# Performance work log

Measured on AMD Instinct MI355X. Metric: run time of the kernel, lower is better.

The kernel has to match this reference:

```python
import jax, jax.numpy as jnp
import numpy as np

B, T, D_IN, H = 128, 1024, 64, 512
EPS = 1e-5


def _layernorm(x, gamma, beta):
    mu = jnp.mean(x, axis=-1, keepdims=True)
    var = jnp.mean(jnp.square(x - mu), axis=-1, keepdims=True)
    return (x - mu) * jax.lax.rsqrt(var + EPS) * gamma + beta


def setup_inputs() -> dict:
    key = jax.random.key(0)
    ks = jax.random.split(key, 10)
    s_in = 1.0 / np.sqrt(D_IN)
    s_h = 1.0 / np.sqrt(H)
    return {
        "x": jax.random.normal(ks[0], (B, T, D_IN), dtype=jnp.float32),
        # layer 0: input_dim -> hidden
        "Wi0": jax.random.uniform(ks[1], (D_IN, H), jnp.float32, -s_in, s_in),
        "bi0": jax.random.uniform(ks[2], (H,), jnp.float32, -s_in, s_in),
        "Wh0": jax.random.uniform(ks[3], (H, H), jnp.float32, -s_h, s_h),
        "bh0": jax.random.uniform(ks[4], (H,), jnp.float32, -s_h, s_h),
        "g0": jnp.ones((H,), jnp.float32),
        "be0": jnp.zeros((H,), jnp.float32),
        # layer 1: hidden -> hidden
        "Wi1": jax.random.uniform(ks[5], (H, H), jnp.float32, -s_h, s_h),
        "bi1": jax.random.uniform(ks[6], (H,), jnp.float32, -s_h, s_h),
        "Wh1": jax.random.uniform(ks[7], (H, H), jnp.float32, -s_h, s_h),
        "bh1": jax.random.uniform(ks[8], (H,), jnp.float32, -s_h, s_h),
        "g1": jnp.ones((H,), jnp.float32),
        "be1": jnp.zeros((H,), jnp.float32),
        # output head: hidden -> 1
        "Wfc": jax.random.uniform(ks[9], (H, 1), jnp.float32, -s_h, s_h),
        "bfc": jnp.zeros((1,), jnp.float32),
    }


def reference(x, Wi0, bi0, Wh0, bh0, g0, be0, Wi1, bi1, Wh1, bh1, g1, be1, Wfc, bfc):
    def step(carry, x_t):
        h0, h1 = carry
        # layer 0: tanh(x W + h W) + residual + LayerNorm
        cand0 = jnp.tanh(x_t @ Wi0 + bi0 + h0 @ Wh0 + bh0)
        h0n = _layernorm(cand0 + h0, g0, be0)
        # layer 1
        cand1 = jnp.tanh(h0n @ Wi1 + bi1 + h1 @ Wh1 + bh1)
        h1n = _layernorm(cand1 + h1, g1, be1)
        return (h0n, h1n), None

    h_init = (jnp.zeros((x.shape[0], Wh0.shape[0]), x.dtype),
              jnp.zeros((x.shape[0], Wh1.shape[0]), x.dtype))
    xs = jnp.swapaxes(x, 0, 1)  # [T, B, D]
    (h0, h1), _ = jax.lax.scan(step, h_init, xs)
    return h1 @ Wfc + bfc  # [B, 1]
```

## Files before the change

### kernel.cpp

```cpp
#include <hip/hip_runtime.h>


#define T_SZ 1024
#define DD   64
#define HH   512
#define NCH  8
#define NBLK 16

typedef __attribute__((ext_vector_type(8))) short short8;
typedef __attribute__((ext_vector_type(4))) float f32x4;
typedef unsigned long long ull;

__device__ __forceinline__ unsigned short f2b(float f) {
  unsigned u = __float_as_uint(f);
  u += 0x7fffu + ((u >> 16) & 1u);
  return (unsigned short)(u >> 16);
}
__device__ __forceinline__ float b2f(unsigned short s) {
  return __uint_as_float(((unsigned)s) << 16);
}
__device__ __forceinline__ ull packf2(float a, float b) {
  return (ull)__float_as_uint(a) | ((ull)__float_as_uint(b) << 32);
}
__device__ __forceinline__ float unpack_lo(ull u) { return __uint_as_float((unsigned)u); }
__device__ __forceinline__ float unpack_hi(ull u) { return __uint_as_float((unsigned)(u >> 32)); }
__device__ __forceinline__ void st_rlx(ull* p, ull v) {
  __hip_atomic_store(p, v, __ATOMIC_RELAXED, __HIP_MEMORY_SCOPE_AGENT);
}
__device__ __forceinline__ ull ld_rlx(const ull* p) {
  return __hip_atomic_load(p, __ATOMIC_RELAXED, __HIP_MEMORY_SCOPE_AGENT);
}
__device__ __forceinline__ unsigned ld_flag(const unsigned* p) {
  return __hip_atomic_load(p, __ATOMIC_RELAXED, __HIP_MEMORY_SCOPE_AGENT);
}
__device__ __forceinline__ void st_flag(unsigned* p, unsigned v) {
  asm volatile("" ::: "memory");
  __hip_atomic_store(p, v, __ATOMIC_RELAXED, __HIP_MEMORY_SCOPE_AGENT);
}
__device__ __forceinline__ float fast_tanh(float z) {
  const float e = __builtin_amdgcn_exp2f(z * 2.885390081777927f);
  return 1.f - 2.f * __builtin_amdgcn_rcpf(e + 1.f);
}

__global__ void prep_kernel(const float* __restrict__ Wh0, const float* __restrict__ Wi1,
                            const float* __restrict__ Wh1,
                            const float* __restrict__ bi0, const float* __restrict__ bh0,
                            const float* __restrict__ bi1, const float* __restrict__ bh1,
                            const float* __restrict__ g0, const float* __restrict__ be0,
                            const float* __restrict__ g1, const float* __restrict__ be1,
                            float* __restrict__ cvec, unsigned* __restrict__ flags) {
  int g = blockIdx.x * blockDim.x + threadIdx.x;
  if (g < HH) {
    float uw0 = 0.f, qw0 = 0.f, uw1 = 0.f, qw1 = 0.f, uh1 = 0.f, qh1 = 0.f;
    for (int j = 0; j < HH; ++j) {
      float a = Wh0[j * HH + g], b = Wi1[j * HH + g], d = Wh1[j * HH + g];
      uw0 += g0[j] * a; qw0 += be0[j] * a;
      uw1 += g0[j] * b; qw1 += be0[j] * b;
      uh1 += g1[j] * d; qh1 += be1[j] * d;
    }
    float b0 = bi0[g] + bh0[g], b1 = bi1[g] + bh1[g];
    cvec[0 * HH + g] = b0 + qw0;
    cvec[1 * HH + g] = b0;
    cvec[2 * HH + g] = b1 + qw1 + qh1;
    cvec[3 * HH + g] = b1 + qw1;
    cvec[4 * HH + g] = uw0;
    cvec[5 * HH + g] = uw1;
    cvec[6 * HH + g] = uh1;
  }
  if (g < 4096) flags[g] = 0;
}

__global__ __launch_bounds__(512, 1) void rnn_mfma(
    const float* __restrict__ x,
    const float* __restrict__ Wi0, const float* __restrict__ Wh0,
    const float* __restrict__ Wi1, const float* __restrict__ Wh1,
    const float* __restrict__ cvec,
    const float* __restrict__ g0v, const float* __restrict__ be0v,
    const float* __restrict__ g1v, const float* __restrict__ be1v,
    const float* __restrict__ wfc, const float* __restrict__ bfc,
    ull* __restrict__ pay, ull* __restrict__ pst,
    unsigned* __restrict__ flags, float* __restrict__ out) {

  const int blk = blockIdx.x, group = blk >> 4, p = blk & 15;
  const int tid = threadIdx.x;
  const int wave = tid >> 6, lane = tid & 63;
  const int quad = lane >> 4, m16 = lane & 15;

  __shared__ unsigned short a0bf[16][536];
  __shared__ unsigned short a1bf[16][536];
  __shared__ unsigned short xsb[16][72];
  __shared__ float partsA[8][8][33];
  __shared__ float partsB[8][8][33];
  __shared__ float partsC[8][8][33];
  __shared__ float partsX[2][8][33];
  __shared__ float2 st0[NCH][NBLK];
  __shared__ float2 st1[NCH][NBLK];

  for (int i = tid; i < 16 * 536; i += 512) {
    (&a0bf[0][0])[i] = 0; (&a1bf[0][0])[i] = 0;
  }
  for (int i = tid; i < 16 * 72; i += 512) (&xsb[0][0])[i] = 0;
  if (tid < NCH * NBLK) {
    (&st0[0][0])[tid] = make_float2(0.f, 0.f);
    (&st1[0][0])[tid] = make_float2(0.f, 0.f);
  }
  {
    float xv = x[((size_t)(group * NCH + wave) * T_SZ) * DD + lane];
    xsb[wave][lane] = f2b(xv);
  }

  short8 wf0[2][2], wfA[2][2], wfB[2][2], wfx[2];
#pragma unroll
  for (int n = 0; n < 2; ++n)
#pragma unroll
    for (int j = 0; j < 8; ++j) wfx[n][j] = 0;
#pragma unroll
  for (int sl = 0; sl < 2; ++sl)
#pragma unroll
    for (int n = 0; n < 2; ++n) {
      const int col = p * 32 + n * 16 + m16;
#pragma unroll
      for (int j = 0; j < 8; ++j) {
        const int k = wave * 64 + sl * 32 + quad * 8 + j;
        wf0[sl][n][j] = (short)f2b(g0v[k] * Wh0[(size_t)k * HH + col]);
        wfA[sl][n][j] = (short)f2b(g0v[k] * Wi1[(size_t)k * HH + col]);
        wfB[sl][n][j] = (short)f2b(g1v[k] * Wh1[(size_t)k * HH + col]);
      }
    }
  if (wave < 2) {
#pragma unroll
    for (int n = 0; n < 2; ++n) {
      const int col = p * 32 + n * 16 + m16;
#pragma unroll
      for (int j = 0; j < 8; ++j)
        wfx[n][j] = (short)f2b(Wi0[(size_t)(wave * 32 + quad * 8 + j) * HH + col]);
    }
  }

  const int cl    = lane & 31;
  const int ech   = ((wave & 3) << 1) + (lane >> 5);
  const int col_e = p * 32 + cl;
  const float c0f = cvec[col_e],          c0i = cvec[HH + col_e];
  const float c1f = cvec[2 * HH + col_e], c1i = cvec[3 * HH + col_e];
  const float uw0 = cvec[4 * HH + col_e], uw1 = cvec[5 * HH + col_e];
  const float uh1 = cvec[6 * HH + col_e];
  const float g0c = g0v[col_e], be0c = be0v[col_e];
  const float g1c = g1v[col_e], be1c = be1v[col_e];

  const int Lp = (wave >= 4) ? 1 : 0;
  ull* const pubpay0 = pay + ((((size_t)blk * 2 + Lp) * 2 + 0) * NCH + ech) * 8 + (cl >> 2);
  ull* const pubpay1 = pubpay0 + (size_t)NCH * 8;
  ull* const pubpst0 = pst + (((size_t)blk * 2 + Lp) * 2 + 0) * NCH + ech;
  ull* const pubpst1 = pubpst0 + NCH;
  unsigned short* const ep_lds = &((wave < 4) ? a0bf : a1bf)[ech][p * 32 + cl];

  const int j0   = 2 * wave;
  const bool two = (j0 + 1 < 15);
  const int pg0  = j0 + (j0 >= p);
  const int pg1  = two ? ((j0 + 1) + ((j0 + 1) >= p)) : pg0;
  const unsigned* pf0 = flags + (group * NBLK + pg0) * 16;
  const unsigned* pf1 = flags + (group * NBLK + pg1) * 16;

  const ull* gp0[5]; const ull* gp1[5]; ull* glw[5]; bool gv[5], gva0[5];
#pragma unroll
  for (int k = 0; k < 5; ++k) {
    const int li  = lane + (k << 6);
    const int lim = two ? 288 : 144;
    const int jr  = (li >= 144) ? 1 : 0;
    const int r2  = li - 144 * jr;
    const int pl  = jr ? pg1 : pg0;
    gv[k]  = (li < lim);
    gva0[k] = gv[k] && (r2 < 72);
    const int L  = (r2 >= 72) ? 1 : 0;
    const int rr = r2 - 72 * L;
    const size_t pb = ((size_t)(group * NBLK + pl) * 2 + L) * 2;
    if (rr < 64) {
      gp0[k] = pay + ((pb + 0) * NCH + (rr >> 3)) * 8 + (rr & 7);
      gp1[k] = pay + ((pb + 1) * NCH + (rr >> 3)) * 8 + (rr & 7);
      glw[k] = (ull*)&(L ? a1bf : a0bf)[rr >> 3][pl * 32 + 4 * (rr & 7)];
    } else {
      gp0[k] = pst + (pb + 0) * NCH + (rr - 64);
      gp1[k] = pst + (pb + 1) * NCH + (rr - 64);
      glw[k] = (ull*)&(L ? st1 : st0)[rr - 64][pl];
    }
  }

  const float* xptr = x + ((size_t)(group * NCH + wave) * T_SZ + 1) * DD + lane;

  float v2prev0 = 0.f, v2prev1 = 0.f;
  float myS0 = 0.f, myQ0 = 0.f, myS1 = 0.f, myQ1 = 0.f;
  __syncthreads();

  for (int s = 0; s <= T_SZ; ++s) {
    const int par = s & 1;

    float m0 = 0.f, r0 = 0.f, m1p = 0.f, r1p = 0.f;
    if (s > 0) {
      float S = 0.f, Q = 0.f;
#pragma unroll
      for (int i = 0; i < NBLK; ++i) { float2 sq = st0[ech][i]; S += sq.x; Q += sq.y; }
      m0 = S * (1.f / HH);
      r0 = __builtin_amdgcn_rsqf(Q * (1.f / HH) - m0 * m0 + 1e-5f);
    }
    if (wave >= 4 && s > 1) {
      float S = 0.f, Q = 0.f;
#pragma unroll
      for (int i = 0; i < NBLK; ++i) { float2 sq = st1[ech][i]; S += sq.x; Q += sq.y; }
      m1p = S * (1.f / HH);
      r1p = __builtin_amdgcn_rsqf(Q * (1.f / HH) - m1p * m1p + 1e-5f);
    }

    {
      f32x4 aA0 = {0.f,0.f,0.f,0.f}, aA1 = {0.f,0.f,0.f,0.f};
      f32x4 aB0 = {0.f,0.f,0.f,0.f}, aB1 = {0.f,0.f,0.f,0.f};
      f32x4 aC0 = {0.f,0.f,0.f,0.f}, aC1 = {0.f,0.f,0.f,0.f};
#pragma unroll
      for (int sl = 0; sl < 2; ++sl) {
        const short8 af0 = *(const short8*)&a0bf[m16][wave * 64 + sl * 32 + quad * 8];
        const short8 af1 = *(const short8*)&a1bf[m16][wave * 64 + sl * 32 + quad * 8];
        aA0 = __builtin_amdgcn_mfma_f32_16x16x32_bf16(af0, wf0[sl][0], aA0, 0, 0, 0);
        aA1 = __builtin_amdgcn_mfma_f32_16x16x32_bf16(af0, wf0[sl][1], aA1, 0, 0, 0);
        aC0 = __builtin_amdgcn_mfma_f32_16x16x32_bf16(af0, wfA[sl][0], aC0, 0, 0, 0);
        aC1 = __builtin_amdgcn_mfma_f32_16x16x32_bf16(af0, wfA[sl][1], aC1, 0, 0, 0);
        aB0 = __builtin_amdgcn_mfma_f32_16x16x32_bf16(af1, wfB[sl][0], aB0, 0, 0, 0);
        aB1 = __builtin_amdgcn_mfma_f32_16x16x32_bf16(af1, wfB[sl][1], aB1, 0, 0, 0);
      }
      if (lane < 32) {
#pragma unroll
        for (int r = 0; r < 4; ++r) {
          partsA[wave][quad * 4 + r][m16]      = aA0[r];
          partsA[wave][quad * 4 + r][16 + m16] = aA1[r];
          partsB[wave][quad * 4 + r][m16]      = aB0[r];
          partsB[wave][quad * 4 + r][16 + m16] = aB1[r];
          partsC[wave][quad * 4 + r][m16]      = aC0[r];
          partsC[wave][quad * 4 + r][16 + m16] = aC1[r];
        }
      }
      if (wave < 2) {
        f32x4 ax0 = {0.f,0.f,0.f,0.f}, ax1 = {0.f,0.f,0.f,0.f};
        const short8 xf = *(const short8*)&xsb[m16][wave * 32 + quad * 8];
        ax0 = __builtin_amdgcn_mfma_f32_16x16x32_bf16(xf, wfx[0], ax0, 0, 0, 0);
        ax1 = __builtin_amdgcn_mfma_f32_16x16x32_bf16(xf, wfx[1], ax1, 0, 0, 0);
        if (lane < 32) {
#pragma unroll
          for (int r = 0; r < 4; ++r) {
            partsX[wave][quad * 4 + r][m16]      = ax0[r];
            partsX[wave][quad * 4 + r][16 + m16] = ax1[r];
          }
        }
      }
    }
    __syncthreads();

    if (wave < 4) {
      if (s < T_SZ) {
        float sH = 0.f;
#pragma unroll
        for (int w = 0; w < 8; ++w) sH += partsA[w][ech][cl];
        const float sX = partsX[0][ech][cl] + partsX[1][ech][cl];
        const float z = ((s == 0) ? c0i : c0f) + r0 * sH - r0 * m0 * uw0 + sX;
        const float h0prev = (s == 0) ? 0.f : (v2prev0 - m0) * r0 * g0c + be0c;
        const float v2 = fast_tanh(z) + h0prev;
        v2prev0 = v2;
        const unsigned vb = f2b(v2);
        *ep_lds = (unsigned short)vb;
        const unsigned u01 = vb | (__shfl_down(vb, 1) << 16);
        const unsigned u23 = __shfl_down(u01, 2);
        if ((cl & 3) == 0)
          st_rlx((par ? pubpay1 : pubpay0), (ull)u01 | ((ull)u23 << 32));
        float S = v2, Q = v2 * v2;
#pragma unroll
        for (int off = 16; off; off >>= 1) {
          S += __shfl_down(S, off, 32); Q += __shfl_down(Q, off, 32);
        }
        if (cl == 0) {
          myS0 = S; myQ0 = Q;
          st_rlx((par ? pubpst1 : pubpst0), packf2(S, Q));
        }
      }
    } else if (s >= 1) {
      float sB = 0.f, sC = 0.f;
#pragma unroll
      for (int w = 0; w < 8; ++w) { sB += partsB[w][ech][cl]; sC += partsC[w][ech][cl]; }
      const float z = ((s == 1) ? c1i : c1f) + r0 * sC - r0 * m0 * uw1
                      + r1p * sB - r1p * m1p * uh1;
      const float h1prev = (s == 1) ? 0.f : (v2prev1 - m1p) * r1p * g1c + be1c;
      const float v2 = fast_tanh(z) + h1prev;
      v2prev1 = v2;
      const unsigned vb = f2b(v2);
      *ep_lds = (unsigned short)vb;
      const unsigned u01 = vb | (__shfl_down(vb, 1) << 16);
      const unsigned u23 = __shfl_down(u01, 2);
      if ((cl & 3) == 0)
        st_rlx((par ? pubpay1 : pubpay0), (ull)u01 | ((ull)u23 << 32));
      float S = v2, Q = v2 * v2;
#pragma unroll
      for (int off = 16; off; off >>= 1) {
        S += __shfl_down(S, off, 32); Q += __shfl_down(Q, off, 32);
      }
      if (cl == 0) {
        myS1 = S; myQ1 = Q;
        st_rlx((par ? pubpst1 : pubpst0), packf2(S, Q));
      }
    }
    __syncthreads();
    if (tid == 0) st_flag(flags + blk * 16, (unsigned)(s + 1));
    if (s == T_SZ) break;

    if (cl == 0) {
      if (wave < 4)       st0[ech][p] = make_float2(myS0, myQ0);
      else if (s >= 1)    st1[ech][p] = make_float2(myS1, myQ1);
    }
    float xv = 0.f;
    if (s + 1 < T_SZ) xv = *xptr;
    xptr += DD;

    if (two) {
      while (ld_flag(pf0) < (unsigned)(s + 1) || ld_flag(pf1) < (unsigned)(s + 1))
        __builtin_amdgcn_s_sleep(1);
    } else {
      while (ld_flag(pf0) < (unsigned)(s + 1)) __builtin_amdgcn_s_sleep(1);
    }

    {
      ull tv[5];
#pragma unroll
      for (int k = 0; k < 5; ++k) {
        const bool v = s ? gv[k] : gva0[k];
        tv[k] = 0;
        if (v) tv[k] = ld_rlx(par ? gp1[k] : gp0[k]);
      }
#pragma unroll
      for (int k = 0; k < 5; ++k) {
        const bool v = s ? gv[k] : gva0[k];
        if (v) *glw[k] = tv[k];
      }
    }
    if (s + 1 < T_SZ) xsb[wave][lane] = f2b(xv);
    __syncthreads();
  }

  if (p == 0) {
    if (tid < 16) {
      const unsigned* pf = flags + (group * NBLK + tid) * 16;
      while (ld_flag(pf) < (unsigned)(T_SZ + 1)) __builtin_amdgcn_s_sleep(1);
    }
    __syncthreads();
    const int c = wave;
    ull su = 0;
    if (lane < 16)
      su = ld_rlx(pst + (((size_t)(group * NBLK + lane) * 2 + 1) * 2 + 0) * NCH + c);
    float S = unpack_lo(su), Q = unpack_hi(su);
#pragma unroll
    for (int off = 32; off; off >>= 1) { S += __shfl_down(S, off); Q += __shfl_down(Q, off); }
    S = __shfl(S, 0); Q = __shfl(Q, 0);
    const float m1 = S * (1.f / HH);
    const float r1 = 1.f / sqrtf(Q * (1.f / HH) - m1 * m1 + 1e-5f);
    float o = 0.f;
#pragma unroll
    for (int it = 0; it < 2; ++it) {
      const int j2 = lane * 2 + it, pl = j2 >> 3, j = j2 & 7;
      ull u = ld_rlx(pay + ((((size_t)(group * NBLK + pl) * 2 + 1) * 2 + 0) * NCH + c) * 8 + j);
#pragma unroll
      for (int q = 0; q < 4; ++q) {
        const int col = pl * 32 + 4 * j + q;
        const float h = (b2f((unsigned short)(u >> (16 * q))) - m1) * r1 * g1v[col] + be1v[col];
        o += h * wfc[col];
      }
    }
#pragma unroll
    for (int off = 32; off; off >>= 1) o += __shfl_down(o, off);
    if (lane == 0) out[group * NCH + c] = o + bfc[0];
  }
}

extern "C" void kernel_launch(void* const* d_in, const int* in_sizes, int n_in,
                              void* d_out, int out_size, void* d_ws, size_t ws_size,
                              hipStream_t stream) {
  const float* x   = (const float*)d_in[0];
  const float* Wi0 = (const float*)d_in[1];
  const float* bi0 = (const float*)d_in[2];
  const float* Wh0 = (const float*)d_in[3];
  const float* bh0 = (const float*)d_in[4];
  const float* g0  = (const float*)d_in[5];
  const float* be0 = (const float*)d_in[6];
  const float* Wi1 = (const float*)d_in[7];
  const float* bi1 = (const float*)d_in[8];
  const float* Wh1 = (const float*)d_in[9];
  const float* bh1 = (const float*)d_in[10];
  const float* g1  = (const float*)d_in[11];
  const float* be1 = (const float*)d_in[12];
  const float* Wfc = (const float*)d_in[13];
  const float* bfc = (const float*)d_in[14];
  float* out = (float*)d_out;

  char* ws = (char*)d_ws;
  float* cvec     = (float*)(ws);
  ull* pay        = (ull*)(ws + 16384);
  ull* pst        = (ull*)(ws + 16384 + 524288);
  unsigned* flags = (unsigned*)(ws + 16384 + 524288 + 65536);

  prep_kernel<<<256, 256, 0, stream>>>(Wh0, Wi1, Wh1, bi0, bh0, bi1, bh1,
                                       g0, be0, g1, be1, cvec, flags);
  rnn_mfma<<<256, 512, 0, stream>>>(x, Wi0, Wh0, Wi1, Wh1, cvec,
                                    g0, be0, g1, be1, Wfc, bfc,
                                    pay, pst, flags, out);
}
```

Baseline: 3.159 ms.

## Replace step flags with sentinel-valued per-consumer mailboxes for inter-block exchange

Removes the per-step flag counters and the extra __syncthreads before publishing. Each producer now writes its hidden-state payload and LayerNorm stats into 16 per-consumer slots. Consumers poll each slot until it no longer holds a sentinel value, then reset it to the sentinel after reading. The goal is to cut one barrier plus a flag round-trip per timestep, so readiness is detected directly on the data. In exchange each producer issues 16 times as many global stores, the workspace grows, and correctness depends on 64-bit atomic visibility and on real data never equalling the all-ones sentinel.

```diff
diff --git a/kernel.cpp b/kernel.cpp
--- a/kernel.cpp
+++ b/kernel.cpp
@@ -6,6 +6,7 @@
 #define HH   512
 #define NCH  8
 #define NBLK 16
+#define SENT 0xFFFFFFFFFFFFFFFFull
 
 typedef __attribute__((ext_vector_type(8))) short short8;
 typedef __attribute__((ext_vector_type(4))) float f32x4;
@@ -29,13 +30,6 @@
 }
 __device__ __forceinline__ ull ld_rlx(const ull* p) {
   return __hip_atomic_load(p, __ATOMIC_RELAXED, __HIP_MEMORY_SCOPE_AGENT);
-}
-__device__ __forceinline__ unsigned ld_flag(const unsigned* p) {
-  return __hip_atomic_load(p, __ATOMIC_RELAXED, __HIP_MEMORY_SCOPE_AGENT);
-}
-__device__ __forceinline__ void st_flag(unsigned* p, unsigned v) {
-  asm volatile("" ::: "memory");
-  __hip_atomic_store(p, v, __ATOMIC_RELAXED, __HIP_MEMORY_SCOPE_AGENT);
 }
 __device__ __forceinline__ float fast_tanh(float z) {
   const float e = __builtin_amdgcn_exp2f(z * 2.885390081777927f);
@@ -48,7 +42,8 @@
                             const float* __restrict__ bi1, const float* __restrict__ bh1,
                             const float* __restrict__ g0, const float* __restrict__ be0,
                             const float* __restrict__ g1, const float* __restrict__ be1,
-                            float* __restrict__ cvec, unsigned* __restrict__ flags) {
+                            float* __restrict__ cvec,
+                            ull* __restrict__ pay, ull* __restrict__ pst) {
   int g = blockIdx.x * blockDim.x + threadIdx.x;
   if (g < HH) {
     float uw0 = 0.f, qw0 = 0.f, uw1 = 0.f, qw1 = 0.f, uh1 = 0.f, qh1 = 0.f;
@@ -67,7 +62,12 @@
     cvec[5 * HH + g] = uw1;
     cvec[6 * HH + g] = uh1;
   }
-  if (g < 4096) flags[g] = 0;
+  ull* pp = pay + (size_t)g * 16;
+#pragma unroll
+  for (int i = 0; i < 16; ++i) pp[i] = SENT;
+  ull* ps = pst + (size_t)g * 2;
+#pragma unroll
+  for (int i = 0; i < 2; ++i) ps[i] = SENT;
 }
 
 __global__ __launch_bounds__(512, 1) void rnn_mfma(
@@ -79,7 +79,7 @@
     const float* __restrict__ g1v, const float* __restrict__ be1v,
     const float* __restrict__ wfc, const float* __restrict__ bfc,
     ull* __restrict__ pay, ull* __restrict__ pst,
-    unsigned* __restrict__ flags, float* __restrict__ out) {
+    float* __restrict__ out) {
 
   const int blk = blockIdx.x, group = blk >> 4, p = blk & 15;
   const int tid = threadIdx.x;
@@ -148,20 +148,18 @@
   const float g1c = g1v[col_e], be1c = be1v[col_e];
 
   const int Lp = (wave >= 4) ? 1 : 0;
-  ull* const pubpay0 = pay + ((((size_t)blk * 2 + Lp) * 2 + 0) * NCH + ech) * 8 + (cl >> 2);
-  ull* const pubpay1 = pubpay0 + (size_t)NCH * 8;
-  ull* const pubpst0 = pst + (((size_t)blk * 2 + Lp) * 2 + 0) * NCH + ech;
-  ull* const pubpst1 = pubpst0 + NCH;
+  ull* const ppayA = pay + ((((size_t)blk * 2 + Lp) * 2 + 0) * 16) * 64 + ech * 8 + (cl >> 2);
+  ull* const ppayB = pay + ((((size_t)blk * 2 + Lp) * 2 + 1) * 16) * 64 + ech * 8 + (cl >> 2);
+  ull* const ppstA = pst + ((((size_t)blk * 2 + Lp) * 2 + 0) * 16) * 8 + ech;
+  ull* const ppstB = pst + ((((size_t)blk * 2 + Lp) * 2 + 1) * 16) * 8 + ech;
   unsigned short* const ep_lds = &((wave < 4) ? a0bf : a1bf)[ech][p * 32 + cl];
 
   const int j0   = 2 * wave;
   const bool two = (j0 + 1 < 15);
   const int pg0  = j0 + (j0 >= p);
   const int pg1  = two ? ((j0 + 1) + ((j0 + 1) >= p)) : pg0;
-  const unsigned* pf0 = flags + (group * NBLK + pg0) * 16;
-  const unsigned* pf1 = flags + (group * NBLK + pg1) * 16;
-
-  const ull* gp0[5]; const ull* gp1[5]; ull* glw[5]; bool gv[5], gva0[5];
+
+  ull* gp0[5]; ull* gp1[5]; ull* glw[5]; bool gv[5], gva0[5];
 #pragma unroll
   for (int k = 0; k < 5; ++k) {
     const int li  = lane + (k << 6);
@@ -169,18 +167,18 @@
     const int jr  = (li >= 144) ? 1 : 0;
     const int r2  = li - 144 * jr;
     const int pl  = jr ? pg1 : pg0;
-    gv[k]  = (li < lim);
+    gv[k]   = (li < lim);
     gva0[k] = gv[k] && (r2 < 72);
     const int L  = (r2 >= 72) ? 1 : 0;
     const int rr = r2 - 72 * L;
     const size_t pb = ((size_t)(group * NBLK + pl) * 2 + L) * 2;
     if (rr < 64) {
-      gp0[k] = pay + ((pb + 0) * NCH + (rr >> 3)) * 8 + (rr & 7);
-      gp1[k] = pay + ((pb + 1) * NCH + (rr >> 3)) * 8 + (rr & 7);
+      gp0[k] = pay + ((pb + 0) * 16 + p) * 64 + rr;
+      gp1[k] = pay + ((pb + 1) * 16 + p) * 64 + rr;
       glw[k] = (ull*)&(L ? a1bf : a0bf)[rr >> 3][pl * 32 + 4 * (rr & 7)];
     } else {
-      gp0[k] = pst + (pb + 0) * NCH + (rr - 64);
-      gp1[k] = pst + (pb + 1) * NCH + (rr - 64);
+      gp0[k] = pst + ((pb + 0) * 16 + p) * 8 + (rr - 64);
+      gp1[k] = pst + ((pb + 1) * 16 + p) * 8 + (rr - 64);
       glw[k] = (ull*)&(L ? st1 : st0)[rr - 64][pl];
     }
   }
@@ -188,7 +186,6 @@
   const float* xptr = x + ((size_t)(group * NCH + wave) * T_SZ + 1) * DD + lane;
 
   float v2prev0 = 0.f, v2prev1 = 0.f;
-  float myS0 = 0.f, myQ0 = 0.f, myS1 = 0.f, myQ1 = 0.f;
   __syncthreads();
 
   for (int s = 0; s <= T_SZ; ++s) {
@@ -266,16 +263,23 @@
         *ep_lds = (unsigned short)vb;
         const unsigned u01 = vb | (__shfl_down(vb, 1) << 16);
         const unsigned u23 = __shfl_down(u01, 2);
-        if ((cl & 3) == 0)
-          st_rlx((par ? pubpay1 : pubpay0), (ull)u01 | ((ull)u23 << 32));
+        if ((cl & 3) == 0) {
+          const ull v = (ull)u01 | ((ull)u23 << 32);
+          ull* b = par ? ppayB : ppayA;
+#pragma unroll
+          for (int r = 0; r < 16; ++r) st_rlx(b + r * 64, v);
+        }
         float S = v2, Q = v2 * v2;
 #pragma unroll
         for (int off = 16; off; off >>= 1) {
           S += __shfl_down(S, off, 32); Q += __shfl_down(Q, off, 32);
         }
         if (cl == 0) {
-          myS0 = S; myQ0 = Q;
-          st_rlx((par ? pubpst1 : pubpst0), packf2(S, Q));
+          st0[ech][p] = make_float2(S, Q);
+          const ull v = packf2(S, Q);
+          ull* b = par ? ppstB : ppstA;
+#pragma unroll
+          for (int r = 0; r < 16; ++r) st_rlx(b + r * 8, v);
         }
       }
     } else if (s >= 1) {
@@ -291,49 +295,51 @@
       *ep_lds = (unsigned short)vb;
       const unsigned u01 = vb | (__shfl_down(vb, 1) << 16);
       const unsigned u23 = __shfl_down(u01, 2);
-      if ((cl & 3) == 0)
-        st_rlx((par ? pubpay1 : pubpay0), (ull)u01 | ((ull)u23 << 32));
+      if ((cl & 3) == 0) {
+        const ull v = (ull)u01 | ((ull)u23 << 32);
+        ull* b = par ? ppayB : ppayA;
+#pragma unroll
+        for (int r = 0; r < 16; ++r) st_rlx(b + r * 64, v);
+      }
       float S = v2, Q = v2 * v2;
 #pragma unroll
       for (int off = 16; off; off >>= 1) {
         S += __shfl_down(S, off, 32); Q += __shfl_down(Q, off, 32);
       }
       if (cl == 0) {
-        myS1 = S; myQ1 = Q;
-        st_rlx((par ? pubpst1 : pubpst0), packf2(S, Q));
-      }
-    }
-    __syncthreads();
-    if (tid == 0) st_flag(flags + blk * 16, (unsigned)(s + 1));
+        st1[ech][p] = make_float2(S, Q);
+        const ull v = packf2(S, Q);
+        ull* b = par ? ppstB : ppstA;
+#pragma unroll
+        for (int r = 0; r < 16; ++r) st_rlx(b + r * 8, v);
+      }
+    }
     if (s == T_SZ) break;
 
-    if (cl == 0) {
-      if (wave < 4)       st0[ech][p] = make_float2(myS0, myQ0);
-      else if (s >= 1)    st1[ech][p] = make_float2(myS1, myQ1);
-    }
     float xv = 0.f;
     if (s + 1 < T_SZ) xv = *xptr;
     xptr += DD;
 
-    if (two) {
-      while (ld_flag(pf0) < (unsigned)(s + 1) || ld_flag(pf1) < (unsigned)(s + 1))
+    {
+      bool need[5];
+#pragma unroll
+      for (int k = 0; k < 5; ++k) need[k] = s ? gv[k] : gva0[k];
+      for (;;) {
+        bool any = false;
+#pragma unroll
+        for (int k = 0; k < 5; ++k) {
+          if (need[k]) {
+            ull* ap = par ? gp1[k] : gp0[k];
+            const ull v = ld_rlx(ap);
+            if (v != SENT) {
+              need[k] = false;
+              st_rlx(ap, SENT);
+              *glw[k] = v;
+            } else any = true;
+          }
+        }
+        if (!any) break;
         __builtin_amdgcn_s_sleep(1);
-    } else {
-      while (ld_flag(pf0) < (unsigned)(s + 1)) __builtin_amdgcn_s_sleep(1);
-    }
-
-    {
-      ull tv[5];
-#pragma unroll
-      for (int k = 0; k < 5; ++k) {
-        const bool v = s ? gv[k] : gva0[k];
-        tv[k] = 0;
-        if (v) tv[k] = ld_rlx(par ? gp1[k] : gp0[k]);
-      }
-#pragma unroll
-      for (int k = 0; k < 5; ++k) {
-        const bool v = s ? gv[k] : gva0[k];
-        if (v) *glw[k] = tv[k];
       }
     }
     if (s + 1 < T_SZ) xsb[wave][lane] = f2b(xv);
@@ -341,15 +347,18 @@
   }
 
   if (p == 0) {
-    if (tid < 16) {
-      const unsigned* pf = flags + (group * NBLK + tid) * 16;
-      while (ld_flag(pf) < (unsigned)(T_SZ + 1)) __builtin_amdgcn_s_sleep(1);
-    }
     __syncthreads();
     const int c = wave;
     ull su = 0;
-    if (lane < 16)
-      su = ld_rlx(pst + (((size_t)(group * NBLK + lane) * 2 + 1) * 2 + 0) * NCH + c);
+    if (lane < 16) {
+      if (lane == 0) {
+        float2 sq = st1[c][0];
+        su = packf2(sq.x, sq.y);
+      } else {
+        const ull* a = pst + ((((size_t)(group * NBLK + lane) * 2 + 1) * 2 + 0) * 16 + 0) * 8 + c;
+        for (;;) { su = ld_rlx(a); if (su != SENT) break; __builtin_amdgcn_s_sleep(1); }
+      }
+    }
     float S = unpack_lo(su), Q = unpack_hi(su);
 #pragma unroll
     for (int off = 32; off; off >>= 1) { S += __shfl_down(S, off); Q += __shfl_down(Q, off); }
@@ -360,7 +369,13 @@
 #pragma unroll
     for (int it = 0; it < 2; ++it) {
       const int j2 = lane * 2 + it, pl = j2 >> 3, j = j2 & 7;
-      ull u = ld_rlx(pay + ((((size_t)(group * NBLK + pl) * 2 + 1) * 2 + 0) * NCH + c) * 8 + j);
+      ull u;
+      if (pl == 0) {
+        u = *(const ull*)&a1bf[c][4 * j];
+      } else {
+        const ull* a = pay + ((((size_t)(group * NBLK + pl) * 2 + 1) * 2 + 0) * 16 + 0) * 64 + c * 8 + j;
+        for (;;) { u = ld_rlx(a); if (u != SENT) break; __builtin_amdgcn_s_sleep(1); }
+      }
 #pragma unroll
       for (int q = 0; q < 4; ++q) {
         const int col = pl * 32 + 4 * j + q;
@@ -395,14 +410,13 @@
   float* out = (float*)d_out;
 
   char* ws = (char*)d_ws;
-  float* cvec     = (float*)(ws);
-  ull* pay        = (ull*)(ws + 16384);
-  ull* pst        = (ull*)(ws + 16384 + 524288);
-  unsigned* flags = (unsigned*)(ws + 16384 + 524288 + 65536);
+  float* cvec = (float*)(ws);
+  ull* pay    = (ull*)(ws + 16384);
+  ull* pst    = (ull*)(ws + 16384 + 8388608);
 
   prep_kernel<<<256, 256, 0, stream>>>(Wh0, Wi1, Wh1, bi0, bh0, bi1, bh1,
-                                       g0, be0, g1, be1, cvec, flags);
+                                       g0, be0, g1, be1, cvec, pay, pst);
   rnn_mfma<<<256, 512, 0, stream>>>(x, Wi0, Wh0, Wi1, Wh1, cvec,
                                     g0, be0, g1, be1, Wfc, bfc,
-                                    pay, pst, flags, out);
-}
+                                    pay, pst, out);
+}
```

After: 6.654 ms. +110.6%, slower.

## Replace per-block flags with per-wave tags to drop a block barrier

Applied to the files above, without the earlier changes.

Each wave now publishes its own step tag after waiting for its outstanding global stores. Consumers poll the 8 per-wave tags of each peer block with a wave-wide vote, instead of a single block flag written after a __syncthreads. This removes one block-wide barrier per timestep and lets waves publish as soon as their own payload is written. In exchange each step polls more tag words, and the ordering relies on vmcnt waits with relaxed atomics rather than a release store, which may be a correctness risk.

```diff
diff --git a/kernel.cpp b/kernel.cpp
--- a/kernel.cpp
+++ b/kernel.cpp
@@ -29,13 +29,6 @@
 }
 __device__ __forceinline__ ull ld_rlx(const ull* p) {
   return __hip_atomic_load(p, __ATOMIC_RELAXED, __HIP_MEMORY_SCOPE_AGENT);
-}
-__device__ __forceinline__ unsigned ld_flag(const unsigned* p) {
-  return __hip_atomic_load(p, __ATOMIC_RELAXED, __HIP_MEMORY_SCOPE_AGENT);
-}
-__device__ __forceinline__ void st_flag(unsigned* p, unsigned v) {
-  asm volatile("" ::: "memory");
-  __hip_atomic_store(p, v, __ATOMIC_RELAXED, __HIP_MEMORY_SCOPE_AGENT);
 }
 __device__ __forceinline__ float fast_tanh(float z) {
   const float e = __builtin_amdgcn_exp2f(z * 2.885390081777927f);
@@ -48,7 +41,7 @@
                             const float* __restrict__ bi1, const float* __restrict__ bh1,
                             const float* __restrict__ g0, const float* __restrict__ be0,
                             const float* __restrict__ g1, const float* __restrict__ be1,
-                            float* __restrict__ cvec, unsigned* __restrict__ flags) {
+                            float* __restrict__ cvec, ull* __restrict__ tags) {
   int g = blockIdx.x * blockDim.x + threadIdx.x;
   if (g < HH) {
     float uw0 = 0.f, qw0 = 0.f, uw1 = 0.f, qw1 = 0.f, uh1 = 0.f, qh1 = 0.f;
@@ -67,7 +60,7 @@
     cvec[5 * HH + g] = uw1;
     cvec[6 * HH + g] = uh1;
   }
-  if (g < 4096) flags[g] = 0;
+  if (g < 2048) tags[g] = 0;
 }
 
 __global__ __launch_bounds__(512, 1) void rnn_mfma(
@@ -79,7 +72,7 @@
     const float* __restrict__ g1v, const float* __restrict__ be1v,
     const float* __restrict__ wfc, const float* __restrict__ bfc,
     ull* __restrict__ pay, ull* __restrict__ pst,
-    unsigned* __restrict__ flags, float* __restrict__ out) {
+    ull* __restrict__ tags, float* __restrict__ out) {
 
   const int blk = blockIdx.x, group = blk >> 4, p = blk & 15;
   const int tid = threadIdx.x;
@@ -153,13 +146,17 @@
   ull* const pubpst0 = pst + (((size_t)blk * 2 + Lp) * 2 + 0) * NCH + ech;
   ull* const pubpst1 = pubpst0 + NCH;
   unsigned short* const ep_lds = &((wave < 4) ? a0bf : a1bf)[ech][p * 32 + cl];
+  ull* const mytag = tags + blk * 8 + wave;
 
   const int j0   = 2 * wave;
   const bool two = (j0 + 1 < 15);
   const int pg0  = j0 + (j0 >= p);
   const int pg1  = two ? ((j0 + 1) + ((j0 + 1) >= p)) : pg0;
-  const unsigned* pf0 = flags + (group * NBLK + pg0) * 16;
-  const unsigned* pf1 = flags + (group * NBLK + pg1) * 16;
+
+  const bool pollact = (lane < 8) || (two && lane < 16);
+  const int  pwidx   = lane & 7;
+  const int  ppl     = (lane < 8) ? pg0 : pg1;
+  const ull* tagaddr = tags + (size_t)(group * NBLK + ppl) * 8 + pwidx;
 
   const ull* gp0[5]; const ull* gp1[5]; ull* glw[5]; bool gv[5], gva0[5];
 #pragma unroll
@@ -169,7 +166,7 @@
     const int jr  = (li >= 144) ? 1 : 0;
     const int r2  = li - 144 * jr;
     const int pl  = jr ? pg1 : pg0;
-    gv[k]  = (li < lim);
+    gv[k]   = (li < lim);
     gva0[k] = gv[k] && (r2 < 72);
     const int L  = (r2 >= 72) ? 1 : 0;
     const int rr = r2 - 72 * L;
@@ -179,8 +176,8 @@
       gp1[k] = pay + ((pb + 1) * NCH + (rr >> 3)) * 8 + (rr & 7);
       glw[k] = (ull*)&(L ? a1bf : a0bf)[rr >> 3][pl * 32 + 4 * (rr & 7)];
     } else {
-      gp0[k] = pst + (pb + 0) * NCH + (rr - 64);
-      gp1[k] = pst + (pb + 1) * NCH + (rr - 64);
+      gp0[k] = pst + ((pb + 0) * NCH + (rr - 64));
+      gp1[k] = pst + ((pb + 1) * NCH + (rr - 64));
       glw[k] = (ull*)&(L ? st1 : st0)[rr - 64][pl];
     }
   }
@@ -188,7 +185,6 @@
   const float* xptr = x + ((size_t)(group * NCH + wave) * T_SZ + 1) * DD + lane;
 
   float v2prev0 = 0.f, v2prev1 = 0.f;
-  float myS0 = 0.f, myQ0 = 0.f, myS1 = 0.f, myQ1 = 0.f;
   __syncthreads();
 
   for (int s = 0; s <= T_SZ; ++s) {
@@ -274,7 +270,7 @@
           S += __shfl_down(S, off, 32); Q += __shfl_down(Q, off, 32);
         }
         if (cl == 0) {
-          myS0 = S; myQ0 = Q;
+          st0[ech][p] = make_float2(S, Q);
           st_rlx((par ? pubpst1 : pubpst0), packf2(S, Q));
         }
       }
@@ -299,27 +295,27 @@
         S += __shfl_down(S, off, 32); Q += __shfl_down(Q, off, 32);
       }
       if (cl == 0) {
-        myS1 = S; myQ1 = Q;
+        st1[ech][p] = make_float2(S, Q);
         st_rlx((par ? pubpst1 : pubpst0), packf2(S, Q));
       }
     }
-    __syncthreads();
-    if (tid == 0) st_flag(flags + blk * 16, (unsigned)(s + 1));
+
+    asm volatile("s_waitcnt vmcnt(0)" ::: "memory");
+    if (lane == 0) st_rlx(mytag, (ull)(s + 1));
     if (s == T_SZ) break;
 
-    if (cl == 0) {
-      if (wave < 4)       st0[ech][p] = make_float2(myS0, myQ0);
-      else if (s >= 1)    st1[ech][p] = make_float2(myS1, myQ1);
-    }
     float xv = 0.f;
     if (s + 1 < T_SZ) xv = *xptr;
     xptr += DD;
 
-    if (two) {
-      while (ld_flag(pf0) < (unsigned)(s + 1) || ld_flag(pf1) < (unsigned)(s + 1))
+    {
+      const ull target = (ull)(s + 1);
+      const bool mycheck = pollact && !((s == 0) && (pwidx >= 4));
+      for (;;) {
+        bool ok = !mycheck || (ld_rlx(tagaddr) >= target);
+        if (__all(ok)) break;
         __builtin_amdgcn_s_sleep(1);
-    } else {
-      while (ld_flag(pf0) < (unsigned)(s + 1)) __builtin_amdgcn_s_sleep(1);
+      }
     }
 
     {
@@ -341,9 +337,10 @@
   }
 
   if (p == 0) {
-    if (tid < 16) {
-      const unsigned* pf = flags + (group * NBLK + tid) * 16;
-      while (ld_flag(pf) < (unsigned)(T_SZ + 1)) __builtin_amdgcn_s_sleep(1);
+    if (tid < 60) {
+      const int pl = 1 + (tid >> 2), w = 4 + (tid & 3);
+      const ull* a = tags + (size_t)(group * NBLK + pl) * 8 + w;
+      while (ld_rlx(a) < (ull)(T_SZ + 1)) __builtin_amdgcn_s_sleep(2);
     }
     __syncthreads();
     const int c = wave;
@@ -355,7 +352,7 @@
     for (int off = 32; off; off >>= 1) { S += __shfl_down(S, off); Q += __shfl_down(Q, off); }
     S = __shfl(S, 0); Q = __shfl(Q, 0);
     const float m1 = S * (1.f / HH);
-    const float r1 = 1.f / sqrtf(Q * (1.f / HH) - m1 * m1 + 1e-5f);
+    const float r1 = __builtin_amdgcn_rsqf(Q * (1.f / HH) - m1 * m1 + 1e-5f);
     float o = 0.f;
 #pragma unroll
     for (int it = 0; it < 2; ++it) {
@@ -395,14 +392,14 @@
   float* out = (float*)d_out;
 
   char* ws = (char*)d_ws;
-  float* cvec     = (float*)(ws);
-  ull* pay        = (ull*)(ws + 16384);
-  ull* pst        = (ull*)(ws + 16384 + 524288);
-  unsigned* flags = (unsigned*)(ws + 16384 + 524288 + 65536);
+  float* cvec = (float*)(ws);
+  ull* pay    = (ull*)(ws + 16384);
+  ull* pst    = (ull*)(ws + 16384 + 524288);
+  ull* tags   = (ull*)(ws + 16384 + 524288 + 65536);
 
   prep_kernel<<<256, 256, 0, stream>>>(Wh0, Wi1, Wh1, bi0, bh0, bi1, bh1,
-                                       g0, be0, g1, be1, cvec, flags);
+                                       g0, be0, g1, be1, cvec, tags);
   rnn_mfma<<<256, 512, 0, stream>>>(x, Wi0, Wh0, Wi1, Wh1, cvec,
                                     g0, be0, g1, be1, Wfc, bfc,
-                                    pay, pst, flags, out);
-}
+                                    pay, pst, tags, out);
+}
```

After: 4.336 ms. +37.3%, slower.
